# Kernel optimization log

Hardware: AMD Instinct MI355X
Metric: run time of the kernel (lower is better)

## Reference

```python
import jax, jax.numpy as jnp
import numpy as np
from jax import lax

H, W = 2048, 2048  # output_size


def setup_inputs() -> dict:
    key = jax.random.key(0)
    # normalized [ymin, xmin, ymax, xmax] in [0,1]; invalid (min>=max) boxes are
    # naturally skipped by the empty-mask logic, same as the torch `continue`.
    boxes = jax.random.uniform(key, (1024, 4), dtype=jnp.float32)
    return {"boxes": boxes}


def reference(boxes):
    ys = jnp.arange(H, dtype=jnp.int32)  # [H]
    xs = jnp.arange(W, dtype=jnp.int32)  # [W]

    def paint(smap, box):
        # pixel coords: truncate toward zero like torch .long(), then clamp
        y1 = jnp.maximum(0, (box[0] * H).astype(jnp.int32))
        x1 = jnp.maximum(0, (box[1] * W).astype(jnp.int32))
        y2 = jnp.minimum(H, (box[2] * H).astype(jnp.int32))
        x2 = jnp.minimum(W, (box[3] * W).astype(jnp.int32))
        cover = ((ys >= y1) & (ys < y2))[:, None] & ((xs >= x1) & (xs < x2))[None, :]  # [H,W]
        # channel values: [1.0, ymin, xmin, ymax, xmax] (normalized box coords)
        vals = jnp.concatenate([jnp.ones((1,), boxes.dtype), box])  # [5]
        # later boxes overwrite earlier ones inside their rectangle (paint order)
        new_map = jnp.where(cover[None, :, :], vals[:, None, None], smap)
        return new_map, None

    smap0 = jnp.zeros((5, H, W), dtype=boxes.dtype)
    smap, _ = lax.scan(paint, smap0, boxes)
    return smap[None]  # (1, 5, H, W)
```

## Files before the change

kernel.cpp:

```cpp
#include <hip/hip_runtime.h>

#define HH 2048
#define WW 2048
#define NB 1024
#define TW 64
#define TH 16

__global__ __launch_bounds__(256, 4) void paint_kernel(const float4* __restrict__ boxes,
                                                       float* __restrict__ out) {
    __shared__ short sy1[NB], sx1[NB], sy2[NB], sx2[NB];
    __shared__ short slist[NB];
    __shared__ unsigned long long imask[4];
    __shared__ unsigned long long fmask[4];

    const int tid  = threadIdx.x;
    const int lane = tid & 63;
    const int wid  = tid >> 6;
    const int tileX = blockIdx.x * TW;
    const int tileY = blockIdx.y * TH;

    for (int i = tid; i < NB; i += 256) {
        float4 b = boxes[i];
        int y1 = (int)(b.x * (float)HH); y1 = max(y1, 0);
        int x1 = (int)(b.y * (float)WW); x1 = max(x1, 0);
        int y2 = (int)(b.z * (float)HH); y2 = min(y2, HH);
        int x2 = (int)(b.w * (float)WW); x2 = min(x2, WW);
        sy1[i] = (short)y1; sx1[i] = (short)x1;
        sy2[i] = (short)y2; sx2[i] = (short)x2;
    }
    __syncthreads();

    int cnt = 0;
    int lastFull = -1;
    for (int c = 0; c < NB / 256; ++c) {
        int b = c * 256 + tid;
        int y1 = sy1[b], x1 = sx1[b], y2 = sy2[b], x2 = sx2[b];
        bool inter = (y1 < tileY + TH) && (y2 > tileY) &&
                     (x1 < tileX + TW) && (x2 > tileX) &&
                     (y1 < y2) && (x1 < x2);
        bool full  = (y1 <= tileY) && (y2 >= tileY + TH) &&
                     (x1 <= tileX) && (x2 >= tileX + TW);
        unsigned long long mi = __ballot(inter);
        unsigned long long mf = __ballot(full);
        if (lane == 0) { imask[wid] = mi; fmask[wid] = mf; }
        __syncthreads();
        int base = cnt;
        for (int w = 0; w < wid; ++w) base += __popcll(imask[w]);
        if (inter) {
            int off = base + __popcll(mi & ((1ull << lane) - 1ull));
            slist[off] = (short)b;
        }
        int total = 0;
        for (int w = 0; w < 4; ++w) total += __popcll(imask[w]);
        cnt += total;
        for (int w = 3; w >= 0; --w) {
            unsigned long long m = fmask[w];
            if (m) { lastFull = c * 256 + w * 64 + 63 - __clzll(m); break; }
        }
        __syncthreads();
    }

    const int px0 = tileX + (tid & 15) * 4;
    const int py  = tileY + (tid >> 4);

    float vals[5][4];
    for (int k = 0; k < 4; ++k) {
        int px = px0 + k;
        int found = lastFull;
        for (int j = cnt - 1; j >= 0; --j) {
            int bi = slist[j];
            if (bi <= lastFull) break;
            if (py >= sy1[bi] && py < sy2[bi] && px >= sx1[bi] && px < sx2[bi]) {
                found = bi;
                break;
            }
        }
        if (found >= 0) {
            float4 bv = boxes[found];
            vals[0][k] = 1.0f;
            vals[1][k] = bv.x; vals[2][k] = bv.y;
            vals[3][k] = bv.z; vals[4][k] = bv.w;
        } else {
            vals[0][k] = 0.0f; vals[1][k] = 0.0f; vals[2][k] = 0.0f;
            vals[3][k] = 0.0f; vals[4][k] = 0.0f;
        }
    }

    const size_t pbase = (size_t)py * WW + px0;
    #pragma unroll
    for (int c = 0; c < 5; ++c) {
        float4 v = make_float4(vals[c][0], vals[c][1], vals[c][2], vals[c][3]);
        *(float4*)(out + (size_t)c * (HH * WW) + pbase) = v;
    }
}

extern "C" void kernel_launch(void* const* d_in, const int* in_sizes, int n_in,
                              void* d_out, int out_size, void* d_ws, size_t ws_size,
                              hipStream_t stream) {
    const float4* boxes = (const float4*)d_in[0];
    float* out = (float*)d_out;
    dim3 grid(WW / TW, HH / TH);
    dim3 block(256);
    paint_kernel<<<grid, block, 0, stream>>>(boxes, out);
}
```

Before: 109.1 us.

## Enlarge tiles, register-resident box culling, forward scan with 4x4 pixels per thread

Tiles grow from 64x16 to 128x32 and each thread now covers a 4x4 pixel patch. Box coordinates stay in registers, and all four ballot rounds write their masks to shared memory before a single barrier. Boxes at or below the last fully covering box are dropped when the candidate list is compacted, and the list stores packed coordinates. Pixels then take one forward pass over the list instead of a backward search per pixel, and tiles with no partial boxes take a uniform fast path. The aim is to cut barriers and per-block setup cost, at the price of a per-pixel scan that can no longer exit early and more registers per thread.

```diff
diff --git a/kernel.cpp b/kernel.cpp
--- a/kernel.cpp
+++ b/kernel.cpp
@@ -3,15 +3,15 @@
 #define HH 2048
 #define WW 2048
 #define NB 1024
-#define TW 64
-#define TH 16
+#define TW 128
+#define TH 32
 
 __global__ __launch_bounds__(256, 4) void paint_kernel(const float4* __restrict__ boxes,
                                                        float* __restrict__ out) {
-    __shared__ short sy1[NB], sx1[NB], sy2[NB], sx2[NB];
-    __shared__ short slist[NB];
-    __shared__ unsigned long long imask[4];
-    __shared__ unsigned long long fmask[4];
+    __shared__ unsigned long long imaskS[4][4];
+    __shared__ unsigned long long fmaskS[4][4];
+    __shared__ uint2 clist[NB];
+    __shared__ short cidxS[NB];
 
     const int tid  = threadIdx.x;
     const int lane = tid & 63;
@@ -19,78 +19,124 @@
     const int tileX = blockIdx.x * TW;
     const int tileY = blockIdx.y * TH;
 
-    for (int i = tid; i < NB; i += 256) {
-        float4 b = boxes[i];
-        int y1 = (int)(b.x * (float)HH); y1 = max(y1, 0);
-        int x1 = (int)(b.y * (float)WW); x1 = max(x1, 0);
-        int y2 = (int)(b.z * (float)HH); y2 = min(y2, HH);
-        int x2 = (int)(b.w * (float)WW); x2 = min(x2, WW);
-        sy1[i] = (short)y1; sx1[i] = (short)x1;
-        sy2[i] = (short)y2; sx2[i] = (short)x2;
+    int ry1[4], rx1[4], ry2[4], rx2[4];
+    bool rint[4];
+    #pragma unroll
+    for (int c = 0; c < 4; ++c) {
+        float4 bx = boxes[c * 256 + tid];
+        int y1 = max(0, (int)(bx.x * (float)HH));
+        int x1 = max(0, (int)(bx.y * (float)WW));
+        int y2 = min(HH, (int)(bx.z * (float)HH));
+        int x2 = min(WW, (int)(bx.w * (float)WW));
+        ry1[c] = y1; rx1[c] = x1; ry2[c] = y2; rx2[c] = x2;
+        bool valid = (y1 < y2) && (x1 < x2);
+        bool inter = valid && (y1 < tileY + TH) && (y2 > tileY) &&
+                     (x1 < tileX + TW) && (x2 > tileX);
+        bool full  = (y1 <= tileY) && (y2 >= tileY + TH) &&
+                     (x1 <= tileX) && (x2 >= tileX + TW);
+        rint[c] = inter;
+        unsigned long long mi = __ballot(inter);
+        unsigned long long mf = __ballot(full);
+        if (lane == 0) { imaskS[c][wid] = mi; fmaskS[c][wid] = mf; }
     }
     __syncthreads();
 
-    int cnt = 0;
     int lastFull = -1;
-    for (int c = 0; c < NB / 256; ++c) {
-        int b = c * 256 + tid;
-        int y1 = sy1[b], x1 = sx1[b], y2 = sy2[b], x2 = sx2[b];
-        bool inter = (y1 < tileY + TH) && (y2 > tileY) &&
-                     (x1 < tileX + TW) && (x2 > tileX) &&
-                     (y1 < y2) && (x1 < x2);
-        bool full  = (y1 <= tileY) && (y2 >= tileY + TH) &&
-                     (x1 <= tileX) && (x2 >= tileX + TW);
-        unsigned long long mi = __ballot(inter);
-        unsigned long long mf = __ballot(full);
-        if (lane == 0) { imask[wid] = mi; fmask[wid] = mf; }
-        __syncthreads();
-        int base = cnt;
-        for (int w = 0; w < wid; ++w) base += __popcll(imask[w]);
-        if (inter) {
-            int off = base + __popcll(mi & ((1ull << lane) - 1ull));
-            slist[off] = (short)b;
-        }
-        int total = 0;
-        for (int w = 0; w < 4; ++w) total += __popcll(imask[w]);
-        cnt += total;
-        for (int w = 3; w >= 0; --w) {
-            unsigned long long m = fmask[w];
-            if (m) { lastFull = c * 256 + w * 64 + 63 - __clzll(m); break; }
-        }
-        __syncthreads();
-    }
+    #pragma unroll
+    for (int c = 3; c >= 0; --c)
+        #pragma unroll
+        for (int w = 3; w >= 0; --w)
+            if (lastFull < 0) {
+                unsigned long long m = fmaskS[c][w];
+                if (m) lastFull = c * 256 + w * 64 + 63 - __clzll(m);
+            }
 
-    const int px0 = tileX + (tid & 15) * 4;
-    const int py  = tileY + (tid >> 4);
-
-    float vals[5][4];
-    for (int k = 0; k < 4; ++k) {
-        int px = px0 + k;
-        int found = lastFull;
-        for (int j = cnt - 1; j >= 0; --j) {
-            int bi = slist[j];
-            if (bi <= lastFull) break;
-            if (py >= sy1[bi] && py < sy2[bi] && px >= sx1[bi] && px < sx2[bi]) {
-                found = bi;
-                break;
-            }
-        }
-        if (found >= 0) {
-            float4 bv = boxes[found];
-            vals[0][k] = 1.0f;
-            vals[1][k] = bv.x; vals[2][k] = bv.y;
-            vals[3][k] = bv.z; vals[4][k] = bv.w;
-        } else {
-            vals[0][k] = 0.0f; vals[1][k] = 0.0f; vals[2][k] = 0.0f;
-            vals[3][k] = 0.0f; vals[4][k] = 0.0f;
+    int cnt_all = 0;
+    int myoff[4];
+    #pragma unroll
+    for (int c = 0; c < 4; ++c) {
+        #pragma unroll
+        for (int w = 0; w < 4; ++w) {
+            unsigned long long m = imaskS[c][w];
+            int d = lastFull - (c * 256 + w * 64);
+            if (d >= 63) m = 0;
+            else if (d >= 0) m &= (~0ull) << (d + 1);
+            if (w == wid)
+                myoff[c] = cnt_all + __popcll(m & ((1ull << lane) - 1ull));
+            cnt_all += __popcll(m);
         }
     }
 
-    const size_t pbase = (size_t)py * WW + px0;
     #pragma unroll
-    for (int c = 0; c < 5; ++c) {
-        float4 v = make_float4(vals[c][0], vals[c][1], vals[c][2], vals[c][3]);
-        *(float4*)(out + (size_t)c * (HH * WW) + pbase) = v;
+    for (int c = 0; c < 4; ++c) {
+        int b = c * 256 + tid;
+        if (rint[c] && b > lastFull) {
+            clist[myoff[c]] = make_uint2(((unsigned)ry1[c] << 16) | (unsigned)rx1[c],
+                                         ((unsigned)ry2[c] << 16) | (unsigned)rx2[c]);
+            cidxS[myoff[c]] = (short)b;
+        }
+    }
+    __syncthreads();
+
+    const int qx  = tid & 31;
+    const int px0 = tileX + qx * 4;
+    const int ry  = tid >> 5;
+    const int py0 = tileY + ry * 4;
+
+    if (cnt_all == 0) {
+        float4 bv = make_float4(0.f, 0.f, 0.f, 0.f);
+        float on = 0.f;
+        if (lastFull >= 0) { bv = boxes[lastFull]; on = 1.f; }
+        float vals[5] = {on, bv.x, bv.y, bv.z, bv.w};
+        #pragma unroll
+        for (int ch = 0; ch < 5; ++ch) {
+            float4 v = make_float4(vals[ch], vals[ch], vals[ch], vals[ch]);
+            size_t base = (size_t)ch * (HH * WW);
+            #pragma unroll
+            for (int s = 0; s < 4; ++s)
+                *(float4*)(out + base + (size_t)(py0 + s) * WW + px0) = v;
+        }
+    } else {
+        int fnd[4][4];
+        #pragma unroll
+        for (int s = 0; s < 4; ++s)
+            #pragma unroll
+            for (int k = 0; k < 4; ++k) fnd[s][k] = lastFull;
+        for (int j = 0; j < cnt_all; ++j) {
+            uint2 pc = clist[j];
+            int bidx = cidxS[j];
+            int by1 = (int)(pc.x >> 16), bx1 = (int)(pc.x & 0xffff);
+            int by2 = (int)(pc.y >> 16), bx2 = (int)(pc.y & 0xffff);
+            #pragma unroll
+            for (int s = 0; s < 4; ++s) {
+                int py = py0 + s;
+                bool yin = (py >= by1) && (py < by2);
+                #pragma unroll
+                for (int k = 0; k < 4; ++k) {
+                    int px = px0 + k;
+                    if (yin && px >= bx1 && px < bx2) fnd[s][k] = bidx;
+                }
+            }
+        }
+        #pragma unroll
+        for (int s = 0; s < 4; ++s) {
+            float4 v[5];
+            #pragma unroll
+            for (int k = 0; k < 4; ++k) {
+                int f = fnd[s][k];
+                float4 bv = (f >= 0) ? boxes[f] : make_float4(0.f, 0.f, 0.f, 0.f);
+                float on = (f >= 0) ? 1.f : 0.f;
+                ((float*)&v[0])[k] = on;
+                ((float*)&v[1])[k] = bv.x;
+                ((float*)&v[2])[k] = bv.y;
+                ((float*)&v[3])[k] = bv.z;
+                ((float*)&v[4])[k] = bv.w;
+            }
+            size_t pb = (size_t)(py0 + s) * WW + px0;
+            #pragma unroll
+            for (int ch = 0; ch < 5; ++ch)
+                *(float4*)(out + (size_t)ch * (HH * WW) + pb) = v[ch];
+        }
     }
 }
 
```

New measurement: 91.82 us. 15.8% less time.
